# Optimization experiments

Measured on AMD Instinct MI355X. Metric: run time of the kernel, lower is better.

Reference implementation:

```python
import jax, jax.numpy as jnp
import numpy as np

MARGIN = 1.0
EPS = 1e-12


def setup_inputs() -> dict:
    key = jax.random.key(0)
    k1, k2 = jax.random.split(key)
    embeddings = jax.random.normal(k1, (4096, 768), dtype=jnp.float32)
    labels = jax.random.randint(k2, (4096,), 0, 4, dtype=jnp.int64)
    return {"embeddings": embeddings, "labels": labels}


def reference(embeddings, labels):
    # F.normalize(p=2, dim=1): x / max(||x||, eps)
    norm = jnp.linalg.norm(embeddings, axis=1, keepdims=True)
    e = embeddings / jnp.maximum(norm, EPS)

    # Euclidean pairwise distance matrix (not squared)
    dot = e @ e.T                                  # [N, N]
    sq = jnp.diagonal(dot)                         # [N]
    dist = sq[None, :] - 2.0 * dot + sq[:, None]
    dist = jnp.sqrt(jnp.maximum(dist, 0.0) + EPS)  # [N, N]

    # Masks: positives = same label, off-diagonal; negatives = different label
    n = labels.shape[0]
    eq = labels[None, :] == labels[:, None]
    pos_mask = eq & ~jnp.eye(n, dtype=bool)
    neg_mask = ~eq

    # Batch-hard mining: per-anchor hardest positive (masked max) and
    # hardest negative (masked min) -- replaces the per-row Python loop.
    d_ap = jnp.max(jnp.where(pos_mask, dist, -jnp.inf), axis=1)  # [N]
    d_an = jnp.min(jnp.where(neg_mask, dist, jnp.inf), axis=1)   # [N]

    valid = jnp.any(pos_mask, axis=1)  # anchors with at least one positive
    per_anchor = jnp.maximum(d_ap - d_an + MARGIN, 0.0)
    per_anchor = jnp.where(valid, per_anchor, 0.0)
    n_valid = jnp.maximum(jnp.sum(valid.astype(jnp.float32)), 1.0)
    return jnp.sum(per_anchor) / n_valid
```

## Files before the change

### kernel.cpp

```cpp
#include <hip/hip_runtime.h>
#include <math.h>

#define N 4096
#define D 768
#define MARGIN 1.0f
#define NBLK 528

typedef _Float16 half8 __attribute__((ext_vector_type(8)));
typedef _Float16 half4 __attribute__((ext_vector_type(4)));
typedef float f32x4 __attribute__((ext_vector_type(4)));

__device__ __forceinline__ void gl2lds16(const void* g, void* l) {
    __builtin_amdgcn_global_load_lds((const __attribute__((address_space(1))) void*)g,
                                     (__attribute__((address_space(3))) void*)l, 16, 0, 0);
}

__global__ __launch_bounds__(256) void normalize_kernel(const float* __restrict__ x,
                                                        _Float16* __restrict__ e,
                                                        float* __restrict__ sq,
                                                        unsigned* __restrict__ ap_bits,
                                                        unsigned* __restrict__ an_bits,
                                                        unsigned* __restrict__ counter) {
    const int tid = threadIdx.x;
    const int wave = tid >> 6, lane = tid & 63;
    const int row = blockIdx.x * 4 + wave;

    const float4* xr = (const float4*)(x + (size_t)row * D);
    float4 f0 = xr[lane];
    float4 f1 = xr[lane + 64];
    float4 f2 = xr[lane + 128];

    float s = f0.x*f0.x + f0.y*f0.y + f0.z*f0.z + f0.w*f0.w
            + f1.x*f1.x + f1.y*f1.y + f1.z*f1.z + f1.w*f1.w
            + f2.x*f2.x + f2.y*f2.y + f2.z*f2.z + f2.w*f2.w;
    #pragma unroll
    for (int off = 1; off < 64; off <<= 1) s += __shfl_xor(s, off, 64);

    float scale = 1.0f / fmaxf(sqrtf(s), 1e-12f);

    half4* er = (half4*)(e + (size_t)row * D);
    half4 h0 = { (_Float16)(f0.x*scale), (_Float16)(f0.y*scale), (_Float16)(f0.z*scale), (_Float16)(f0.w*scale) };
    half4 h1 = { (_Float16)(f1.x*scale), (_Float16)(f1.y*scale), (_Float16)(f1.z*scale), (_Float16)(f1.w*scale) };
    half4 h2 = { (_Float16)(f2.x*scale), (_Float16)(f2.y*scale), (_Float16)(f2.z*scale), (_Float16)(f2.w*scale) };
    er[lane]       = h0;
    er[lane + 64]  = h1;
    er[lane + 128] = h2;

    if (lane == 0) {
        sq[row] = s * scale * scale;
        ap_bits[row] = 0u;
        an_bits[row] = 0x7f800000u;
    }
    if (blockIdx.x == 0 && tid == 0) *counter = 0u;
}

__global__ __launch_bounds__(256) void mine_kernel(const _Float16* __restrict__ e,
                                                   const float* __restrict__ sq,
                                                   const int* __restrict__ labels,
                                                   unsigned* __restrict__ ap_bits,
                                                   unsigned* __restrict__ an_bits,
                                                   unsigned* __restrict__ counter,
                                                   float* __restrict__ out) {
    __shared__ unsigned short S[8192];

    int bi = 0, rem = blockIdx.x;
    while (rem >= 32 - bi) { rem -= 32 - bi; ++bi; }
    const int bj = bi + rem;
    const int i0 = bi * 128, j0 = bj * 128;

    const int tid  = threadIdx.x;
    const int w    = tid >> 6;
    const int lane = tid & 63;
    const int wi   = (w & 1) * 64;
    const int wj   = (w >> 1) * 64;
    const int ln15 = lane & 15;
    const int lq   = lane >> 4;

    f32x4 acc[4][4] = {};

    for (int k0 = 0; k0 < D; k0 += 32) {
        __syncthreads();
        #pragma unroll
        for (int p = 0; p < 2; ++p) {
            int s  = p * 256 + tid;
            int r  = s >> 2;
            int kg = (s & 3) ^ ((r >> 1) & 3);
            const _Float16* ga = e + (size_t)(i0 + r) * D + k0 + kg * 8;
            const _Float16* gb = e + (size_t)(j0 + r) * D + k0 + kg * 8;
            char* la = (char*)S + (p * 256 + w * 64) * 16;
            char* lb = (char*)S + 8192 + (p * 256 + w * 64) * 16;
            gl2lds16(ga, la);
            gl2lds16(gb, lb);
        }
        __syncthreads();

        half8 af[4], bf[4];
        #pragma unroll
        for (int mt = 0; mt < 4; ++mt) {
            int r  = wi + mt * 16 + ln15;
            int kx = lq ^ ((r >> 1) & 3);
            af[mt] = *(const half8*)&S[r * 32 + kx * 8];
        }
        #pragma unroll
        for (int nt = 0; nt < 4; ++nt) {
            int r  = wj + nt * 16 + ln15;
            int kx = lq ^ ((r >> 1) & 3);
            bf[nt] = *(const half8*)&S[4096 + r * 32 + kx * 8];
        }
        #pragma unroll
        for (int mt = 0; mt < 4; ++mt)
            #pragma unroll
            for (int nt = 0; nt < 4; ++nt)
                acc[mt][nt] = __builtin_amdgcn_mfma_f32_16x16x32_f16(af[mt], bf[nt], acc[mt][nt], 0, 0, 0);
    }

    float sqi[4][4]; int labi[4][4];
    #pragma unroll
    for (int mt = 0; mt < 4; ++mt)
        #pragma unroll
        for (int rg = 0; rg < 4; ++rg) {
            int i = i0 + wi + mt * 16 + lq * 4 + rg;
            sqi[mt][rg] = sq[i];
            labi[mt][rg] = labels[i];
        }
    float sqj[4]; int labj[4];
    #pragma unroll
    for (int nt = 0; nt < 4; ++nt) {
        int j = j0 + wj + nt * 16 + ln15;
        sqj[nt] = sq[j];
        labj[nt] = labels[j];
    }

    float api[4][4], ani[4][4], apj[4], anj[4];
    #pragma unroll
    for (int mt = 0; mt < 4; ++mt)
        #pragma unroll
        for (int rg = 0; rg < 4; ++rg) { api[mt][rg] = -INFINITY; ani[mt][rg] = INFINITY; }
    #pragma unroll
    for (int nt = 0; nt < 4; ++nt) { apj[nt] = -INFINITY; anj[nt] = INFINITY; }

    #pragma unroll
    for (int nt = 0; nt < 4; ++nt) {
        int j = j0 + wj + nt * 16 + ln15;
        #pragma unroll
        for (int mt = 0; mt < 4; ++mt)
            #pragma unroll
            for (int rg = 0; rg < 4; ++rg) {
                int i = i0 + wi + mt * 16 + lq * 4 + rg;
                float d2 = sqi[mt][rg] + sqj[nt] - 2.0f * acc[mt][nt][rg];
                float dist = sqrtf(fmaxf(d2, 0.0f) + 1e-12f);
                if (labi[mt][rg] == labj[nt]) {
                    if (i != j) {
                        api[mt][rg] = fmaxf(api[mt][rg], dist);
                        apj[nt]     = fmaxf(apj[nt], dist);
                    }
                } else {
                    ani[mt][rg] = fminf(ani[mt][rg], dist);
                    anj[nt]     = fminf(anj[nt], dist);
                }
            }
    }

    #pragma unroll
    for (int mt = 0; mt < 4; ++mt)
        #pragma unroll
        for (int rg = 0; rg < 4; ++rg) {
            float a_ = api[mt][rg], n_ = ani[mt][rg];
            #pragma unroll
            for (int off = 1; off < 16; off <<= 1) {
                a_ = fmaxf(a_, __shfl_xor(a_, off, 64));
                n_ = fminf(n_, __shfl_xor(n_, off, 64));
            }
            if (ln15 == 0) {
                int i = i0 + wi + mt * 16 + lq * 4 + rg;
                if (a_ > -1.0e37f) atomicMax(&ap_bits[i], __float_as_uint(a_));
                if (n_ <  1.0e37f) atomicMin(&an_bits[i], __float_as_uint(n_));
            }
        }

    if (bi != bj) {
        #pragma unroll
        for (int nt = 0; nt < 4; ++nt) {
            float a_ = apj[nt], n_ = anj[nt];
            #pragma unroll
            for (int off = 16; off < 64; off <<= 1) {
                a_ = fmaxf(a_, __shfl_xor(a_, off, 64));
                n_ = fminf(n_, __shfl_xor(n_, off, 64));
            }
            if (lq == 0) {
                int j = j0 + wj + nt * 16 + ln15;
                if (a_ > -1.0e37f) atomicMax(&ap_bits[j], __float_as_uint(a_));
                if (n_ <  1.0e37f) atomicMin(&an_bits[j], __float_as_uint(n_));
            }
        }
    }

    __shared__ unsigned lastFlag;
    __syncthreads();
    if (tid == 0) lastFlag = (atomicAdd(counter, 1u) == NBLK - 1) ? 1u : 0u;
    __syncthreads();
    if (!lastFlag) return;

    __shared__ int cnt[4];
    __shared__ float red[8];
    if (tid < 4) cnt[tid] = 0;
    __syncthreads();
    int local[4] = {0, 0, 0, 0};
    for (int i = tid; i < N; i += 256) local[labels[i] & 3]++;
    #pragma unroll
    for (int c = 0; c < 4; c++) atomicAdd(&cnt[c], local[c]);
    __syncthreads();

    float sum = 0.f, nv = 0.f;
    for (int i = tid; i < N; i += 256) {
        int l = labels[i] & 3;
        if (cnt[l] >= 2) {
            nv += 1.f;
            float apv = __uint_as_float(atomicAdd(&ap_bits[i], 0u));
            float anv = __uint_as_float(atomicAdd(&an_bits[i], 0u));
            if (anv < 3.0e38f) sum += fmaxf(apv - anv + MARGIN, 0.f);
        }
    }

    #pragma unroll
    for (int off = 32; off; off >>= 1) {
        sum += __shfl_down(sum, off, 64);
        nv  += __shfl_down(nv,  off, 64);
    }
    if ((tid & 63) == 0) { red[tid >> 6] = sum; red[4 + (tid >> 6)] = nv; }
    __syncthreads();
    if (tid == 0) {
        float s = red[0] + red[1] + red[2] + red[3];
        float n = red[4] + red[5] + red[6] + red[7];
        out[0] = s / fmaxf(n, 1.f);
    }
}

extern "C" void kernel_launch(void* const* d_in, const int* in_sizes, int n_in,
                              void* d_out, int out_size, void* d_ws, size_t ws_size,
                              hipStream_t stream) {
    const float* x = (const float*)d_in[0];
    const int* labels = (const int*)d_in[1];
    float* out = (float*)d_out;

    _Float16* e = (_Float16*)d_ws;
    float* sq = (float*)(e + (size_t)N * D);
    unsigned* ap_bits = (unsigned*)(sq + N);
    unsigned* an_bits = ap_bits + N;
    unsigned* counter = an_bits + N;

    normalize_kernel<<<N / 4, 256, 0, stream>>>(x, e, sq, ap_bits, an_bits, counter);
    mine_kernel<<<NBLK, 256, 0, stream>>>(e, sq, labels, ap_bits, an_bits, counter, out);
}
```

Baseline: 135.8 us.

## Shrink Gram tiles to 64x64 for more blocks and LDS-combine column atomics

Cuts the symmetric tile size from 128 to 64, so 2080 blocks run instead of 528 and each wave computes a 16x64 strip with fewer accumulators. The goal is to fill more of the GPU's CUs and reduce register pressure. Column-side min/max results are first combined in LDS so each block issues one global atomic per column. The final reduction now uses an acquire fence and plain loads instead of atomic reads. In exchange, each block loads A and B tiles with lower reuse, so global and L2 traffic per FLOP goes up.

```diff
diff --git a/kernel.cpp b/kernel.cpp
--- a/kernel.cpp
+++ b/kernel.cpp
@@ -4,7 +4,8 @@
 #define N 4096
 #define D 768
 #define MARGIN 1.0f
-#define NBLK 528
+#define NB 64
+#define NBLK 2080
 
 typedef _Float16 half8 __attribute__((ext_vector_type(8)));
 typedef _Float16 half4 __attribute__((ext_vector_type(4)));
@@ -61,138 +62,135 @@
                                                    unsigned* __restrict__ an_bits,
                                                    unsigned* __restrict__ counter,
                                                    float* __restrict__ out) {
-    __shared__ unsigned short S[8192];
+    __shared__ unsigned short S[4096];
 
     int bi = 0, rem = blockIdx.x;
-    while (rem >= 32 - bi) { rem -= 32 - bi; ++bi; }
+    while (rem >= NB - bi) { rem -= NB - bi; ++bi; }
     const int bj = bi + rem;
-    const int i0 = bi * 128, j0 = bj * 128;
+    const int i0 = bi * 64, j0 = bj * 64;
+    const bool diag = (bi == bj);
 
     const int tid  = threadIdx.x;
     const int w    = tid >> 6;
     const int lane = tid & 63;
-    const int wi   = (w & 1) * 64;
-    const int wj   = (w >> 1) * 64;
     const int ln15 = lane & 15;
     const int lq   = lane >> 4;
-
-    f32x4 acc[4][4] = {};
+    const int wi16 = w * 16;
+
+    f32x4 acc[4] = {};
+
+    const int rs  = tid >> 2;
+    const int kgs = (tid & 3) ^ ((rs >> 1) & 3);
+    const _Float16* gA = e + (size_t)(i0 + rs) * D + kgs * 8;
+    const _Float16* gB = e + (size_t)(j0 + rs) * D + kgs * 8;
+    char* ldsA = (char*)S + w * 1024;
+    char* ldsB = (char*)S + 4096 + w * 1024;
 
     for (int k0 = 0; k0 < D; k0 += 32) {
         __syncthreads();
-        #pragma unroll
-        for (int p = 0; p < 2; ++p) {
-            int s  = p * 256 + tid;
-            int r  = s >> 2;
-            int kg = (s & 3) ^ ((r >> 1) & 3);
-            const _Float16* ga = e + (size_t)(i0 + r) * D + k0 + kg * 8;
-            const _Float16* gb = e + (size_t)(j0 + r) * D + k0 + kg * 8;
-            char* la = (char*)S + (p * 256 + w * 64) * 16;
-            char* lb = (char*)S + 8192 + (p * 256 + w * 64) * 16;
-            gl2lds16(ga, la);
-            gl2lds16(gb, lb);
-        }
-        __syncthreads();
-
-        half8 af[4], bf[4];
-        #pragma unroll
-        for (int mt = 0; mt < 4; ++mt) {
-            int r  = wi + mt * 16 + ln15;
-            int kx = lq ^ ((r >> 1) & 3);
-            af[mt] = *(const half8*)&S[r * 32 + kx * 8];
-        }
+        gl2lds16(gA + k0, ldsA);
+        gl2lds16(gB + k0, ldsB);
+        __syncthreads();
+
+        const int rA  = wi16 + ln15;
+        const int kxA = lq ^ ((rA >> 1) & 3);
+        half8 af = *(const half8*)&S[rA * 32 + kxA * 8];
+        half8 bf[4];
         #pragma unroll
         for (int nt = 0; nt < 4; ++nt) {
-            int r  = wj + nt * 16 + ln15;
-            int kx = lq ^ ((r >> 1) & 3);
-            bf[nt] = *(const half8*)&S[4096 + r * 32 + kx * 8];
-        }
-        #pragma unroll
-        for (int mt = 0; mt < 4; ++mt)
-            #pragma unroll
-            for (int nt = 0; nt < 4; ++nt)
-                acc[mt][nt] = __builtin_amdgcn_mfma_f32_16x16x32_f16(af[mt], bf[nt], acc[mt][nt], 0, 0, 0);
-    }
-
-    float sqi[4][4]; int labi[4][4];
-    #pragma unroll
-    for (int mt = 0; mt < 4; ++mt)
-        #pragma unroll
-        for (int rg = 0; rg < 4; ++rg) {
-            int i = i0 + wi + mt * 16 + lq * 4 + rg;
-            sqi[mt][rg] = sq[i];
-            labi[mt][rg] = labels[i];
-        }
+            int rB = nt * 16 + ln15;
+            int kx = lq ^ ((rB >> 1) & 3);
+            bf[nt] = *(const half8*)&S[2048 + rB * 32 + kx * 8];
+        }
+        #pragma unroll
+        for (int nt = 0; nt < 4; ++nt)
+            acc[nt] = __builtin_amdgcn_mfma_f32_16x16x32_f16(af, bf[nt], acc[nt], 0, 0, 0);
+    }
+
+    float sqi[4]; int labi[4];
+    #pragma unroll
+    for (int rg = 0; rg < 4; ++rg) {
+        int i = i0 + wi16 + lq * 4 + rg;
+        sqi[rg] = sq[i];
+        labi[rg] = labels[i];
+    }
     float sqj[4]; int labj[4];
     #pragma unroll
     for (int nt = 0; nt < 4; ++nt) {
-        int j = j0 + wj + nt * 16 + ln15;
+        int j = j0 + nt * 16 + ln15;
         sqj[nt] = sq[j];
         labj[nt] = labels[j];
     }
 
-    float api[4][4], ani[4][4], apj[4], anj[4];
-    #pragma unroll
-    for (int mt = 0; mt < 4; ++mt)
-        #pragma unroll
-        for (int rg = 0; rg < 4; ++rg) { api[mt][rg] = -INFINITY; ani[mt][rg] = INFINITY; }
+    float api[4], ani[4], apj[4], anj[4];
+    #pragma unroll
+    for (int rg = 0; rg < 4; ++rg) { api[rg] = -INFINITY; ani[rg] = INFINITY; }
     #pragma unroll
     for (int nt = 0; nt < 4; ++nt) { apj[nt] = -INFINITY; anj[nt] = INFINITY; }
 
     #pragma unroll
     for (int nt = 0; nt < 4; ++nt) {
-        int j = j0 + wj + nt * 16 + ln15;
-        #pragma unroll
-        for (int mt = 0; mt < 4; ++mt)
-            #pragma unroll
-            for (int rg = 0; rg < 4; ++rg) {
-                int i = i0 + wi + mt * 16 + lq * 4 + rg;
-                float d2 = sqi[mt][rg] + sqj[nt] - 2.0f * acc[mt][nt][rg];
-                float dist = sqrtf(fmaxf(d2, 0.0f) + 1e-12f);
-                if (labi[mt][rg] == labj[nt]) {
-                    if (i != j) {
-                        api[mt][rg] = fmaxf(api[mt][rg], dist);
-                        apj[nt]     = fmaxf(apj[nt], dist);
-                    }
-                } else {
-                    ani[mt][rg] = fminf(ani[mt][rg], dist);
-                    anj[nt]     = fminf(anj[nt], dist);
+        int j = j0 + nt * 16 + ln15;
+        #pragma unroll
+        for (int rg = 0; rg < 4; ++rg) {
+            int i = i0 + wi16 + lq * 4 + rg;
+            float d2 = sqi[rg] + sqj[nt] - 2.0f * acc[nt][rg];
+            float dist = sqrtf(fmaxf(d2, 0.0f) + 1e-12f);
+            if (labi[rg] == labj[nt]) {
+                if (i != j) {
+                    api[rg] = fmaxf(api[rg], dist);
+                    apj[nt] = fmaxf(apj[nt], dist);
                 }
+            } else {
+                ani[rg] = fminf(ani[rg], dist);
+                anj[nt] = fminf(anj[nt], dist);
             }
-    }
-
-    #pragma unroll
-    for (int mt = 0; mt < 4; ++mt)
-        #pragma unroll
-        for (int rg = 0; rg < 4; ++rg) {
-            float a_ = api[mt][rg], n_ = ani[mt][rg];
-            #pragma unroll
-            for (int off = 1; off < 16; off <<= 1) {
-                a_ = fmaxf(a_, __shfl_xor(a_, off, 64));
-                n_ = fminf(n_, __shfl_xor(n_, off, 64));
-            }
-            if (ln15 == 0) {
-                int i = i0 + wi + mt * 16 + lq * 4 + rg;
-                if (a_ > -1.0e37f) atomicMax(&ap_bits[i], __float_as_uint(a_));
-                if (n_ <  1.0e37f) atomicMin(&an_bits[i], __float_as_uint(n_));
-            }
-        }
-
-    if (bi != bj) {
+        }
+    }
+
+    #pragma unroll
+    for (int rg = 0; rg < 4; ++rg) {
+        float a_ = api[rg], n_ = ani[rg];
+        #pragma unroll
+        for (int off = 1; off < 16; off <<= 1) {
+            a_ = fmaxf(a_, __shfl_xor(a_, off, 64));
+            n_ = fminf(n_, __shfl_xor(n_, off, 64));
+        }
+        if (ln15 == 0) {
+            int i = i0 + wi16 + lq * 4 + rg;
+            if (a_ > 0.0f)    atomicMax(&ap_bits[i], __float_as_uint(a_));
+            if (n_ < 1.0e37f) atomicMin(&an_bits[i], __float_as_uint(n_));
+        }
+    }
+
+    if (!diag) {
         #pragma unroll
         for (int nt = 0; nt < 4; ++nt) {
-            float a_ = apj[nt], n_ = anj[nt];
             #pragma unroll
             for (int off = 16; off < 64; off <<= 1) {
-                a_ = fmaxf(a_, __shfl_xor(a_, off, 64));
-                n_ = fminf(n_, __shfl_xor(n_, off, 64));
+                apj[nt] = fmaxf(apj[nt], __shfl_xor(apj[nt], off, 64));
+                anj[nt] = fminf(anj[nt], __shfl_xor(anj[nt], off, 64));
             }
-            if (lq == 0) {
-                int j = j0 + wj + nt * 16 + ln15;
-                if (a_ > -1.0e37f) atomicMax(&ap_bits[j], __float_as_uint(a_));
-                if (n_ <  1.0e37f) atomicMin(&an_bits[j], __float_as_uint(n_));
+        }
+        __syncthreads();
+        unsigned* jap = (unsigned*)S;
+        unsigned* jan = ((unsigned*)S) + 64;
+        if (tid < 64) { jap[tid] = 0u; jan[tid] = 0x7f800000u; }
+        __syncthreads();
+        if (lq == 0) {
+            #pragma unroll
+            for (int nt = 0; nt < 4; ++nt) {
+                int c = nt * 16 + ln15;
+                if (apj[nt] > 0.0f)    atomicMax(&jap[c], __float_as_uint(apj[nt]));
+                if (anj[nt] < 1.0e37f) atomicMin(&jan[c], __float_as_uint(anj[nt]));
             }
         }
+        __syncthreads();
+        if (tid < 64) {
+            unsigned a = jap[tid], n = jan[tid];
+            if (a != 0u)          atomicMax(&ap_bits[j0 + tid], a);
+            if (n != 0x7f800000u) atomicMin(&an_bits[j0 + tid], n);
+        }
     }
 
     __shared__ unsigned lastFlag;
@@ -200,6 +198,7 @@
     if (tid == 0) lastFlag = (atomicAdd(counter, 1u) == NBLK - 1) ? 1u : 0u;
     __syncthreads();
     if (!lastFlag) return;
+    __builtin_amdgcn_fence(__ATOMIC_ACQUIRE, "agent");
 
     __shared__ int cnt[4];
     __shared__ float red[8];
@@ -216,8 +215,8 @@
         int l = labels[i] & 3;
         if (cnt[l] >= 2) {
             nv += 1.f;
-            float apv = __uint_as_float(atomicAdd(&ap_bits[i], 0u));
-            float anv = __uint_as_float(atomicAdd(&an_bits[i], 0u));
+            float apv = __uint_as_float(ap_bits[i]);
+            float anv = __uint_as_float(an_bits[i]);
             if (anv < 3.0e38f) sum += fmaxf(apv - anv + MARGIN, 0.f);
         }
     }
```

Measured after the change: 137.2 us. No clear change (+1.0%).

## Load MFMA operands directly from global memory, dropping LDS staging

Applied to the files above, without the earlier changes.

Removes the shared-memory staging of the A/B tiles and the two barriers per k-step. Each wave now loads its half8 MFMA fragments straight from global memory (relying on L1/L2 for reuse) and the k-loop is unrolled by 4. Launch bounds add a minimum of 3 blocks per CU. The final reduction replaces atomic reads with an acquire fence plus plain loads, and positive-distance atomics are skipped when the value is not positive. The trade is that the LDS-level data reuse across the four waves is lost, so more global and cache traffic is issued.

```diff
diff --git a/kernel.cpp b/kernel.cpp
--- a/kernel.cpp
+++ b/kernel.cpp
@@ -9,11 +9,6 @@
 typedef _Float16 half8 __attribute__((ext_vector_type(8)));
 typedef _Float16 half4 __attribute__((ext_vector_type(4)));
 typedef float f32x4 __attribute__((ext_vector_type(4)));
-
-__device__ __forceinline__ void gl2lds16(const void* g, void* l) {
-    __builtin_amdgcn_global_load_lds((const __attribute__((address_space(1))) void*)g,
-                                     (__attribute__((address_space(3))) void*)l, 16, 0, 0);
-}
 
 __global__ __launch_bounds__(256) void normalize_kernel(const float* __restrict__ x,
                                                         _Float16* __restrict__ e,
@@ -54,19 +49,18 @@
     if (blockIdx.x == 0 && tid == 0) *counter = 0u;
 }
 
-__global__ __launch_bounds__(256) void mine_kernel(const _Float16* __restrict__ e,
-                                                   const float* __restrict__ sq,
-                                                   const int* __restrict__ labels,
-                                                   unsigned* __restrict__ ap_bits,
-                                                   unsigned* __restrict__ an_bits,
-                                                   unsigned* __restrict__ counter,
-                                                   float* __restrict__ out) {
-    __shared__ unsigned short S[8192];
-
+__global__ __launch_bounds__(256, 3) void mine_kernel(const _Float16* __restrict__ e,
+                                                      const float* __restrict__ sq,
+                                                      const int* __restrict__ labels,
+                                                      unsigned* __restrict__ ap_bits,
+                                                      unsigned* __restrict__ an_bits,
+                                                      unsigned* __restrict__ counter,
+                                                      float* __restrict__ out) {
     int bi = 0, rem = blockIdx.x;
     while (rem >= 32 - bi) { rem -= 32 - bi; ++bi; }
     const int bj = bi + rem;
     const int i0 = bi * 128, j0 = bj * 128;
+    const bool diag = (bi == bj);
 
     const int tid  = threadIdx.x;
     const int w    = tid >> 6;
@@ -76,37 +70,24 @@
     const int ln15 = lane & 15;
     const int lq   = lane >> 4;
 
+    const _Float16* pA[4];
+    const _Float16* pB[4];
+    #pragma unroll
+    for (int mt = 0; mt < 4; ++mt)
+        pA[mt] = e + (size_t)(i0 + wi + mt * 16 + ln15) * D + lq * 8;
+    #pragma unroll
+    for (int nt = 0; nt < 4; ++nt)
+        pB[nt] = e + (size_t)(j0 + wj + nt * 16 + ln15) * D + lq * 8;
+
     f32x4 acc[4][4] = {};
 
+    #pragma unroll 4
     for (int k0 = 0; k0 < D; k0 += 32) {
-        __syncthreads();
-        #pragma unroll
-        for (int p = 0; p < 2; ++p) {
-            int s  = p * 256 + tid;
-            int r  = s >> 2;
-            int kg = (s & 3) ^ ((r >> 1) & 3);
-            const _Float16* ga = e + (size_t)(i0 + r) * D + k0 + kg * 8;
-            const _Float16* gb = e + (size_t)(j0 + r) * D + k0 + kg * 8;
-            char* la = (char*)S + (p * 256 + w * 64) * 16;
-            char* lb = (char*)S + 8192 + (p * 256 + w * 64) * 16;
-            gl2lds16(ga, la);
-            gl2lds16(gb, lb);
-        }
-        __syncthreads();
-
         half8 af[4], bf[4];
         #pragma unroll
-        for (int mt = 0; mt < 4; ++mt) {
-            int r  = wi + mt * 16 + ln15;
-            int kx = lq ^ ((r >> 1) & 3);
-            af[mt] = *(const half8*)&S[r * 32 + kx * 8];
-        }
-        #pragma unroll
-        for (int nt = 0; nt < 4; ++nt) {
-            int r  = wj + nt * 16 + ln15;
-            int kx = lq ^ ((r >> 1) & 3);
-            bf[nt] = *(const half8*)&S[4096 + r * 32 + kx * 8];
-        }
+        for (int mt = 0; mt < 4; ++mt) af[mt] = *(const half8*)(pA[mt] + k0);
+        #pragma unroll
+        for (int nt = 0; nt < 4; ++nt) bf[nt] = *(const half8*)(pB[nt] + k0);
         #pragma unroll
         for (int mt = 0; mt < 4; ++mt)
             #pragma unroll
@@ -173,12 +154,12 @@
             }
             if (ln15 == 0) {
                 int i = i0 + wi + mt * 16 + lq * 4 + rg;
-                if (a_ > -1.0e37f) atomicMax(&ap_bits[i], __float_as_uint(a_));
-                if (n_ <  1.0e37f) atomicMin(&an_bits[i], __float_as_uint(n_));
-            }
-        }
-
-    if (bi != bj) {
+                if (a_ > 0.0f)    atomicMax(&ap_bits[i], __float_as_uint(a_));
+                if (n_ < 1.0e37f) atomicMin(&an_bits[i], __float_as_uint(n_));
+            }
+        }
+
+    if (!diag) {
         #pragma unroll
         for (int nt = 0; nt < 4; ++nt) {
             float a_ = apj[nt], n_ = anj[nt];
@@ -189,8 +170,8 @@
             }
             if (lq == 0) {
                 int j = j0 + wj + nt * 16 + ln15;
-                if (a_ > -1.0e37f) atomicMax(&ap_bits[j], __float_as_uint(a_));
-                if (n_ <  1.0e37f) atomicMin(&an_bits[j], __float_as_uint(n_));
+                if (a_ > 0.0f)    atomicMax(&ap_bits[j], __float_as_uint(a_));
+                if (n_ < 1.0e37f) atomicMin(&an_bits[j], __float_as_uint(n_));
             }
         }
     }
@@ -200,6 +181,7 @@
     if (tid == 0) lastFlag = (atomicAdd(counter, 1u) == NBLK - 1) ? 1u : 0u;
     __syncthreads();
     if (!lastFlag) return;
+    __builtin_amdgcn_fence(__ATOMIC_ACQUIRE, "agent");
 
     __shared__ int cnt[4];
     __shared__ float red[8];
@@ -216,8 +198,8 @@
         int l = labels[i] & 3;
         if (cnt[l] >= 2) {
             nv += 1.f;
-            float apv = __uint_as_float(atomicAdd(&ap_bits[i], 0u));
-            float anv = __uint_as_float(atomicAdd(&an_bits[i], 0u));
+            float apv = __uint_as_float(ap_bits[i]);
+            float anv = __uint_as_float(an_bits[i]);
             if (anv < 3.0e38f) sum += fmaxf(apv - anv + MARGIN, 0.f);
         }
     }
```

Measured after the change: 163.0 us. +20.0%, slower.
